# Optimization experiments

Measured on AMD Instinct MI355X. Metric: run time of the kernel, lower is better.

Reference implementation:

```python
import jax, jax.numpy as jnp
import numpy as np

D = 1024      # embedding_dim
H = 16        # n_heads
HD = D // H   # head_dim = 64
E = 8         # num_experts
K = 2         # top_k
I = 1024      # moe intermediate
S = 2048      # seq_len
B = 1
EPS = 1e-6
THETA = 10000.0


def _rmsnorm(x, w):
    xf = x.astype(jnp.float32)
    var = jnp.mean(xf * xf, axis=-1, keepdims=True)
    return (xf * jax.lax.rsqrt(var + EPS)).astype(x.dtype) * w


def _rope(x, positions):
    # x: [B, S, H, HD], neox-style rotate-half RoPE
    half = HD // 2
    inv_freq = 1.0 / (THETA ** (jnp.arange(0, half, dtype=jnp.float32) / half))
    freqs = positions.astype(jnp.float32)[:, None] * inv_freq[None, :]  # [S, half]
    cos = jnp.cos(freqs)[None, :, None, :]
    sin = jnp.sin(freqs)[None, :, None, :]
    x1, x2 = x[..., :half], x[..., half:]
    return jnp.concatenate([x1 * cos - x2 * sin, x1 * sin + x2 * cos], axis=-1).astype(x.dtype)


def _attn(x, positions, wqkv, wo):
    b, s, _ = x.shape
    qkv = (x @ wqkv).reshape(b, s, 3, H, HD)
    q, k, v = qkv[:, :, 0], qkv[:, :, 1], qkv[:, :, 2]
    q = _rope(q, positions)
    k = _rope(k, positions)
    scale = 1.0 / np.sqrt(HD)
    scores = jnp.einsum('bqhd,bkhd->bhqk', q, k) * scale
    causal = jnp.tril(jnp.ones((s, s), dtype=bool))
    scores = jnp.where(causal[None, None], scores, jnp.finfo(scores.dtype).min)
    probs = jax.nn.softmax(scores, axis=-1)
    o = jnp.einsum('bhqk,bkhd->bqhd', probs, v).reshape(b, s, D)
    return o @ wo


def _moe(x, gate_w, wg, wu, wd):
    # x: [T, D]
    T = x.shape[0]
    logits = x @ gate_w                                    # [T, E]
    probs = jax.nn.softmax(logits.astype(jnp.float32), axis=-1)
    vals, idx = jax.lax.top_k(probs, K)                    # [T, K]
    vals = vals / jnp.sum(vals, axis=-1, keepdims=True)    # renormalize=True
    combine = jnp.zeros((T, E), dtype=jnp.float32)
    combine = combine.at[jnp.arange(T)[:, None], idx].add(vals)
    combine = combine.astype(x.dtype)                      # [T, E]
    out = jnp.zeros_like(x)
    for e in range(E):  # fixed small expert loop; SwiGLU expert FFN
        h = jax.nn.silu(x @ wg[e]) * (x @ wu[e])
        out = out + combine[:, e:e + 1] * (h @ wd[e])
    return out


def setup_inputs() -> dict:
    key = jax.random.key(0)
    ks = jax.random.split(key, 8)
    std = 0.02
    return {
        'positions': jnp.arange(S, dtype=jnp.int32),
        'hidden_states': jax.random.normal(ks[0], (B, S, D), jnp.float32),
        'residual': jax.random.normal(ks[1], (B, S, D), jnp.float32),
        'ln1_w': jnp.ones((D,), jnp.float32),
        'ln2_w': jnp.ones((D,), jnp.float32),
        'wqkv': jax.random.normal(ks[2], (D, 3 * D), jnp.float32) * std,
        'wo': jax.random.normal(ks[3], (D, D), jnp.float32) * std,
        'gate_w': jax.random.normal(ks[4], (D, E), jnp.float32) * std,
        'wg': jax.random.normal(ks[5], (E, D, I), jnp.float32) * std,
        'wu': jax.random.normal(ks[6], (E, D, I), jnp.float32) * std,
        'wd': jax.random.normal(ks[7], (E, I, D), jnp.float32) * std,
    }


def reference(positions, hidden_states, residual, ln1_w, ln2_w, wqkv, wo, gate_w, wg, wu, wd):
    # _forward_with_post_attn_norm: residual arg is overwritten by hidden_states
    res = hidden_states
    x = _rmsnorm(hidden_states, ln1_w)
    x = res + _attn(x, positions, wqkv, wo)
    res2 = x
    y = _rmsnorm(x, ln2_w)
    b, s, _ = y.shape
    moe_out = _moe(y.reshape(-1, D), gate_w, wg, wu, wd).reshape(b, s, D)
    return res2 + moe_out
```

## Files before the change

### kernel.cpp

```cpp
#include <hip/hip_runtime.h>
#include <math.h>

constexpr int S  = 2048;
constexpr int D  = 1024;
constexpr int NH = 16;
constexpr int NE = 8;
constexpr float EPS   = 1e-6f;
constexpr float THETA = 10000.0f;
constexpr float SCL2  = 0.125f * 1.4426950408889634f;
constexpr float LOG2E = 1.4426950408889634f;

typedef unsigned short u16;
typedef unsigned int   u32;
typedef unsigned long long u64;
typedef __attribute__((ext_vector_type(8))) short short8;
typedef __attribute__((ext_vector_type(4))) float f32x4;

__device__ __forceinline__ u16 f2bf(float x) {
  union { float f; u32 u; } v; v.f = x;
  u32 r = (v.u + 0x7FFFu + ((v.u >> 16) & 1u)) >> 16;
  return (u16)r;
}
__device__ __forceinline__ float bf2f(u16 h) {
  union { u32 u; float f; } v; v.u = ((u32)h) << 16;
  return v.f;
}
__device__ __forceinline__ f32x4 mfma16(short8 a, short8 b, f32x4 c) {
  return __builtin_amdgcn_mfma_f32_16x16x32_bf16(a, b, c, 0, 0, 0);
}
__device__ __forceinline__ void gl_lds16(const void* g, void* l) {
  __builtin_amdgcn_global_load_lds((const __attribute__((address_space(1))) u32*)g,
                                   (__attribute__((address_space(3))) u32*)l, 16, 0, 0);
}
__device__ __forceinline__ u64 pack4bf(float a, float b, float c, float d) {
  return (u64)f2bf(a) | ((u64)f2bf(b) << 16) | ((u64)f2bf(c) << 32) | ((u64)f2bf(d) << 48);
}

__global__ __launch_bounds__(256) void prep_kernel(const float* __restrict__ wqkv,
    const float* __restrict__ wo, const float* __restrict__ wg, const float* __restrict__ wu,
    const float* __restrict__ wd, const int* __restrict__ positions,
    const float* __restrict__ hidden, const float* __restrict__ ln1_w,
    u16* __restrict__ wqkvT2, u16* __restrict__ woT2, u16* __restrict__ wgT,
    u16* __restrict__ wuT, u16* __restrict__ wdT, float2* __restrict__ ropetab,
    u16* __restrict__ xn2, int* __restrict__ counts) {
  const int b = blockIdx.x;
  const int tid = threadIdx.x;
  if (b >= 7424) {
    const int t = b - 7424;
    const float* xr = hidden + (size_t)t * D;
    float v[4]; float ss = 0.f;
#pragma unroll
    for (int i = 0; i < 4; ++i) { v[i] = xr[tid + i * 256]; ss += v[i] * v[i]; }
#pragma unroll
    for (int m = 32; m >= 1; m >>= 1) ss += __shfl_xor(ss, m, 64);
    __shared__ float red[4];
    if ((tid & 63) == 0) red[tid >> 6] = ss;
    __syncthreads();
    const float rs = rsqrtf((red[0] + red[1] + red[2] + red[3]) * (1.f / (float)D) + EPS);
#pragma unroll
    for (int i = 0; i < 4; ++i) {
      const int d = tid + i * 256;
      const float y = v[i] * rs * ln1_w[d];
      const u16 h = f2bf(y);
      xn2[(size_t)t * 2048 + d] = h;
      xn2[(size_t)t * 2048 + 1024 + d] = f2bf(y - bf2f(h));
    }
    return;
  }
  if (b >= 7168) {
    if (b == 7168 && tid < 8) counts[tid] = 0;
    const int idx = (b - 7168) * 256 + tid;
    const int t = idx >> 5, p = idx & 31;
    const float inv = powf(THETA, -(float)p * (1.f / 32.f));
    const float fr = (float)positions[t] * inv;
    float sn, cs; sincosf(fr, &sn, &cs);
    ropetab[idx] = make_float2(cs, sn);
    return;
  }
  __shared__ float t_[64][65];
  const float* W; u16* out; int N, n0, k0; bool split;
  if (b < 768) {
    W = wqkv; out = wqkvT2; N = 3072; split = true;
    n0 = (b % 48) * 64; k0 = (b / 48) * 64;
  } else if (b < 1024) {
    W = wo; out = woT2; N = 1024; split = true;
    const int r = b - 768; n0 = (r & 15) * 64; k0 = (r >> 4) * 64;
  } else {
    int r;
    if (b < 3072)      { r = b - 1024; const int e = r >> 8; W = wg + (size_t)e * 1048576; out = wgT + (size_t)e * 1048576; }
    else if (b < 5120) { r = b - 3072; const int e = r >> 8; W = wu + (size_t)e * 1048576; out = wuT + (size_t)e * 1048576; }
    else               { r = b - 5120; const int e = r >> 8; W = wd + (size_t)e * 1048576; out = wdT + (size_t)e * 1048576; }
    N = 1024; split = false;
    r &= 255; n0 = (r & 15) * 64; k0 = (r >> 4) * 64;
  }
  const int rr = tid >> 4, c4 = (tid & 15) * 4;
#pragma unroll
  for (int i = 0; i < 4; ++i) {
    const float4 v = *(const float4*)(W + (size_t)(k0 + rr + i * 16) * N + n0 + c4);
    t_[rr + i * 16][c4 + 0] = v.x; t_[rr + i * 16][c4 + 1] = v.y;
    t_[rr + i * 16][c4 + 2] = v.z; t_[rr + i * 16][c4 + 3] = v.w;
  }
  __syncthreads();
  if (split) {
#pragma unroll
    for (int i = 0; i < 4; ++i) {
      const int n = n0 + rr + i * 16;
      u16* oh = out + (size_t)n * 2048 + k0 + c4;
      const float v0 = t_[c4 + 0][rr + i * 16], v1 = t_[c4 + 1][rr + i * 16];
      const float v2 = t_[c4 + 2][rr + i * 16], v3 = t_[c4 + 3][rr + i * 16];
      *(u64*)(void*)oh = pack4bf(v0, v1, v2, v3);
      *(u64*)(void*)(oh + 1024) = pack4bf(v0 - bf2f(f2bf(v0)), v1 - bf2f(f2bf(v1)),
                                          v2 - bf2f(f2bf(v2)), v3 - bf2f(f2bf(v3)));
    }
  } else {
#pragma unroll
    for (int i = 0; i < 4; ++i) {
      const int n = n0 + rr + i * 16;
      u16* o = out + (size_t)n * 1024 + k0 + c4;
      *(u64*)(void*)o = pack4bf(t_[c4 + 0][rr + i * 16], t_[c4 + 1][rr + i * 16],
                                t_[c4 + 2][rr + i * 16], t_[c4 + 3][rr + i * 16]);
    }
  }
}

__global__ __launch_bounds__(256) void gemm_qkv(const u16* __restrict__ A2,
    const u16* __restrict__ Bt2, float* __restrict__ Cpart) {
  __shared__ u16 As[2][128 * 32];
  __shared__ u16 Bs[2][128 * 32];
  const int b = blockIdx.x;
  const int xcd = b & 7, ii = b >> 3;
  const int m0 = (ii & 15) * 128;
  const int np = (ii >> 4) % 3, ks = (ii >> 4) / 3;
  const int n0 = (xcd * 3 + np) * 128;
  const int kk0 = ks * 48, kk1 = kk0 + 48;
  const int tid = threadIdx.x, wv = tid >> 6, lane = tid & 63;
  const int l15 = lane & 15, lg = lane >> 4;
  const int wr = wv >> 1, wc = wv & 1;
  const int sr = lane >> 2, sk = (lane & 3) * 16;
  const u16* aptr[2]; const u16* bptr[2];
#pragma unroll
  for (int i = 0; i < 2; ++i) {
    aptr[i] = A2 + (size_t)(m0 + (wv * 2 + i) * 16 + sr) * 2048;
    bptr[i] = Bt2 + (size_t)(n0 + (wv * 2 + i) * 16 + sr) * 2048;
  }
  auto STAGE = [&](int buf, int kk) {
    const int t = kk * 32;
    int ka, kb;
    if (t < 1024)      { ka = t;        kb = t; }
    else if (t < 2048) { ka = t;        kb = t - 1024; }
    else               { ka = t - 2048; kb = t - 1024; }
#pragma unroll
    for (int i = 0; i < 2; ++i) {
      gl_lds16((const char*)(aptr[i] + ka) + sk, (char*)As + buf * 8192 + (wv * 2 + i) * 1024);
      gl_lds16((const char*)(bptr[i] + kb) + sk, (char*)Bs + buf * 8192 + (wv * 2 + i) * 1024);
    }
  };
  f32x4 acc[4][4] = {};
  STAGE(0, kk0);
  __syncthreads();
  int cur = 0;
  for (int kk = kk0; kk < kk1; ++kk) {
    if (kk + 1 < kk1) STAGE(cur ^ 1, kk + 1);
    const u16* Ab = (const u16*)As + cur * 4096;
    const u16* Bb = (const u16*)Bs + cur * 4096;
    short8 a[4], bb[4];
#pragma unroll
    for (int i = 0; i < 4; ++i)
      a[i] = *(const short8*)(const void*)(Ab + (size_t)(wr * 64 + i * 16 + l15) * 32 + lg * 8);
#pragma unroll
    for (int j = 0; j < 4; ++j)
      bb[j] = *(const short8*)(const void*)(Bb + (size_t)(wc * 64 + j * 16 + l15) * 32 + lg * 8);
    __builtin_amdgcn_s_setprio(1);
#pragma unroll
    for (int i = 0; i < 4; ++i)
#pragma unroll
      for (int j = 0; j < 4; ++j) acc[i][j] = mfma16(a[i], bb[j], acc[i][j]);
    __builtin_amdgcn_s_setprio(0);
    __syncthreads();
    cur ^= 1;
  }
  float* P = Cpart + (size_t)ks * S * 3072;
#pragma unroll
  for (int i = 0; i < 4; ++i)
#pragma unroll
    for (int j = 0; j < 4; ++j)
#pragma unroll
      for (int r = 0; r < 4; ++r) {
        const int row = m0 + wr * 64 + i * 16 + lg * 4 + r;
        const int col = n0 + wc * 64 + j * 16 + l15;
        P[(size_t)row * 3072 + col] = acc[i][j][r];
      }
}

__global__ __launch_bounds__(256) void qkv_combine(const float* __restrict__ Cp,
    const float2* __restrict__ tab, u16* __restrict__ Ch, u16* __restrict__ Cl) {
  const int t = blockIdx.x, tid = threadIdx.x;
  const float* r0 = Cp + (size_t)t * 3072;
  const float* r1 = r0 + (size_t)S * 3072;
  const size_t ob = (size_t)t * 3072;
#pragma unroll
  for (int i = 0; i < 4; ++i) {
    const int pi = tid + i * 256;
    const int h = pi >> 5, p = pi & 31;
    const int col = h * 64 + p;
    const float x1 = r0[col] + r1[col];
    const float x2 = r0[col + 32] + r1[col + 32];
    const float2 cs = tab[t * 32 + p];
    const float y1 = x1 * cs.x - x2 * cs.y;
    const float y2 = x1 * cs.y + x2 * cs.x;
    const u16 h1 = f2bf(y1);
    Ch[ob + col] = h1; Cl[ob + col] = f2bf(y1 - bf2f(h1));
    const u16 h2 = f2bf(y2);
    Ch[ob + col + 32] = h2; Cl[ob + col + 32] = f2bf(y2 - bf2f(h2));
  }
#pragma unroll
  for (int i = 0; i < 4; ++i) {
    const int col = 2048 + tid + i * 256;
    const float y = r0[col] + r1[col];
    const u16 h = f2bf(y);
    Ch[ob + col] = h; Cl[ob + col] = f2bf(y - bf2f(h));
  }
}

__global__ __launch_bounds__(256) void gemm_wo(const u16* __restrict__ A2,
    const u16* __restrict__ Bt2, float* __restrict__ Pout) {
  constexpr int N = 1024;
  __shared__ u16 As[2][128 * 32];
  __shared__ u16 Bs[2][128 * 32];
  const int b = blockIdx.x;
  const int xcd = b & 7, ii = b >> 3;
  const int n0 = xcd * 128;
  const int m0 = (ii & 15) * 128;
  const int ks = ii >> 4;
  const int kk0 = ks * 24, kk1 = kk0 + 24;
  const int tid = threadIdx.x, wv = tid >> 6, lane = tid & 63;
  const int l15 = lane & 15, lg = lane >> 4;
  const int wr = wv >> 1, wc = wv & 1;
  const int sr = lane >> 2, sk = (lane & 3) * 16;
  const u16* aptr[2]; const u16* bptr[2];
#pragma unroll
  for (int i = 0; i < 2; ++i) {
    aptr[i] = A2 + (size_t)(m0 + (wv * 2 + i) * 16 + sr) * 2048;
    bptr[i] = Bt2 + (size_t)(n0 + (wv * 2 + i) * 16 + sr) * 2048;
  }
  auto STAGE = [&](int buf, int kk) {
    const int t = kk * 32;
    int ka, kb;
    if (t < 1024)      { ka = t;        kb = t; }
    else if (t < 2048) { ka = t;        kb = t - 1024; }
    else               { ka = t - 2048; kb = t - 1024; }
#pragma unroll
    for (int i = 0; i < 2; ++i) {
      gl_lds16((const char*)(aptr[i] + ka) + sk, (char*)As + buf * 8192 + (wv * 2 + i) * 1024);
      gl_lds16((const char*)(bptr[i] + kb) + sk, (char*)Bs + buf * 8192 + (wv * 2 + i) * 1024);
    }
  };
  f32x4 acc[4][4] = {};
  STAGE(0, kk0);
  __syncthreads();
  int cur = 0;
  for (int kk = kk0; kk < kk1; ++kk) {
    if (kk + 1 < kk1) STAGE(cur ^ 1, kk + 1);
    const u16* Ab = (const u16*)As + cur * 4096;
    const u16* Bb = (const u16*)Bs + cur * 4096;
    short8 a[4], bb[4];
#pragma unroll
    for (int i = 0; i < 4; ++i)
      a[i] = *(const short8*)(const void*)(Ab + (size_t)(wr * 64 + i * 16 + l15) * 32 + lg * 8);
#pragma unroll
    for (int j = 0; j < 4; ++j)
      bb[j] = *(const short8*)(const void*)(Bb + (size_t)(wc * 64 + j * 16 + l15) * 32 + lg * 8);
    __builtin_amdgcn_s_setprio(1);
#pragma unroll
    for (int i = 0; i < 4; ++i)
#pragma unroll
      for (int j = 0; j < 4; ++j) acc[i][j] = mfma16(a[i], bb[j], acc[i][j]);
    __builtin_amdgcn_s_setprio(0);
    __syncthreads();
    cur ^= 1;
  }
  float* P = Pout + (size_t)ks * S * N;
#pragma unroll
  for (int i = 0; i < 4; ++i)
#pragma unroll
    for (int j = 0; j < 4; ++j)
#pragma unroll
      for (int r = 0; r < 4; ++r) {
        const int row = m0 + wr * 64 + i * 16 + lg * 4 + r;
        const int col = n0 + wc * 64 + j * 16 + l15;
        P[(size_t)row * N + col] = acc[i][j][r];
      }
}

__global__ __launch_bounds__(256, 3) void attn_mfma(const u16* __restrict__ Qh,
    const u16* __restrict__ Ql, float* __restrict__ Opart, float2* __restrict__ ml) {
  const int b = blockIdx.x;
  const int head = (b & 7) + 8 * ((b >> 3) & 1);
  const int qb = 31 - ((b >> 4) & 31);
  const int sp = (b >> 9) & 3;
  const int q0 = qb * 64;
  const int ktiles = qb + 1;
  const int kbase = ktiles >> 2, krem = ktiles & 3;
  const int t0 = sp * kbase + (sp < krem ? sp : krem);
  const int t1 = t0 + kbase + (sp < krem ? 1 : 0);
  const int tid = threadIdx.x, w = tid >> 6, lane = tid & 63;
  const int l15 = lane & 15, lg = lane >> 4;
  __shared__ u16 Kh[64 * 64];
  __shared__ u16 Kl[64 * 64];
  __shared__ __align__(16) u16 Vth[64 * 72];
  __shared__ __align__(16) u16 Vtl[64 * 72];
  __shared__ __align__(16) u16 Pp[4][16 * 72];

  short8 qh[2], qlo[2];
  {
    const size_t qbase = (size_t)(q0 + w * 16 + l15) * 3072 + head * 64;
    qh[0]  = *(const short8*)(const void*)(Qh + qbase + lg * 8);
    qh[1]  = *(const short8*)(const void*)(Qh + qbase + 32 + lg * 8);
    qlo[0] = *(const short8*)(const void*)(Ql + qbase + lg * 8);
    qlo[1] = *(const short8*)(const void*)(Ql + qbase + 32 + lg * 8);
  }
  f32x4 oacc[4] = {};
  float m_run = -__builtin_inff(), l_run = 0.f;
  const int qrow0 = q0 + w * 16 + lg * 4;
  const int qcol  = q0 + w * 16 + l15;

  const int vhl = tid >> 7, rem = tid & 127;
  const int vkq = rem & 15, vdg = rem >> 4;
  const u16* vbase = (vhl ? Ql : Qh) + 2048 + head * 64 + vdg * 8;
  u16* vdst = vhl ? Vtl : Vth;
  short8 vr[4];

  auto STAGEK = [&](int kt) {
#pragma unroll
    for (int i = 0; i < 2; ++i) {
      const int inst = w * 2 + i;
      const int key = inst * 8 + (lane >> 3);
      const int db = ((lane & 7) * 16) ^ ((key & 7) << 4);
      gl_lds16((const char*)(Qh + (size_t)(kt * 64 + key) * 3072 + 1024 + head * 64) + db,
               (char*)Kh + inst * 1024);
      gl_lds16((const char*)(Ql + (size_t)(kt * 64 + key) * 3072 + 1024 + head * 64) + db,
               (char*)Kl + inst * 1024);
    }
  };
  auto VLOAD = [&](int kt) {
    const u16* vs = vbase + (size_t)(kt * 64 + vkq * 4) * 3072;
    vr[0] = *(const short8*)(const void*)vs;
    vr[1] = *(const short8*)(const void*)(vs + 3072);
    vr[2] = *(const short8*)(const void*)(vs + 6144);
    vr[3] = *(const short8*)(const void*)(vs + 9216);
  };
  auto VWRITE = [&]() {
#pragma unroll
    for (int jj = 0; jj < 8; ++jj) {
      const u64 pk = (u64)(u16)vr[0][jj] | ((u64)(u16)vr[1][jj] << 16) |
                     ((u64)(u16)vr[2][jj] << 32) | ((u64)(u16)vr[3][jj] << 48);
      *(u64*)(void*)(vdst + (vdg * 8 + jj) * 72 + vkq * 4) = pk;
    }
  };

  if (t0 < t1) {
    STAGEK(t0);
    VLOAD(t0);
    VWRITE();
    __syncthreads();
  }
  for (int t = t0; t < t1; ++t) {
    const int k0 = t * 64;
    const bool more = (t + 1 < t1);
    f32x4 sacc[4];
    __builtin_amdgcn_s_setprio(1);
#pragma unroll
    for (int nt = 0; nt < 4; ++nt) {
      const int key = nt * 16 + l15;
      const char* kbh = (const char*)Kh + key * 128;
      const char* kbl = (const char*)Kl + key * 128;
      const int sw = (key & 7) << 4;
      const short8 kh0 = *(const short8*)(const void*)(kbh + ((lg * 16) ^ sw));
      const short8 kh1 = *(const short8*)(const void*)(kbh + ((64 + lg * 16) ^ sw));
      const short8 kl0 = *(const short8*)(const void*)(kbl + ((lg * 16) ^ sw));
      const short8 kl1 = *(const short8*)(const void*)(kbl + ((64 + lg * 16) ^ sw));
      f32x4 s = {};
      s = mfma16(kh0, qh[0], s);  s = mfma16(kh1, qh[1], s);
      s = mfma16(kh0, qlo[0], s); s = mfma16(kh1, qlo[1], s);
      s = mfma16(kl0, qh[0], s);  s = mfma16(kl1, qh[1], s);
      sacc[nt] = s;
    }
    __builtin_amdgcn_s_setprio(0);
    __syncthreads();
    if (more) { STAGEK(t + 1); VLOAD(t + 1); }
#pragma unroll
    for (int nt = 0; nt < 4; ++nt)
#pragma unroll
      for (int r = 0; r < 4; ++r) sacc[nt][r] *= SCL2;
    if (t == qb) {
#pragma unroll
      for (int nt = 0; nt < 4; ++nt) {
        const int keyb = k0 + nt * 16 + lg * 4;
#pragma unroll
        for (int r = 0; r < 4; ++r)
          if (keyb + r > qcol) sacc[nt][r] = -__builtin_inff();
      }
    }
    float mx = sacc[0][0];
#pragma unroll
    for (int nt = 0; nt < 4; ++nt)
#pragma unroll
      for (int r = 0; r < 4; ++r) mx = fmaxf(mx, sacc[nt][r]);
    mx = fmaxf(mx, __shfl_xor(mx, 16, 64));
    mx = fmaxf(mx, __shfl_xor(mx, 32, 64));
    const bool grow = mx > m_run + 8.f;
    if (__any(grow)) {
      const float m_new = fmaxf(m_run, mx);
      const float fac = __builtin_amdgcn_exp2f(m_run - m_new);
      m_run = m_new;
      l_run *= fac;
      float facB[4];
#pragma unroll
      for (int r = 0; r < 4; ++r) facB[r] = __shfl(fac, lg * 4 + r, 64);
#pragma unroll
      for (int nd = 0; nd < 4; ++nd)
#pragma unroll
        for (int r = 0; r < 4; ++r) oacc[nd][r] *= facB[r];
    }
    float ls = 0.f;
#pragma unroll
    for (int nt = 0; nt < 4; ++nt)
#pragma unroll
      for (int r = 0; r < 4; ++r) {
        sacc[nt][r] = __builtin_amdgcn_exp2f(sacc[nt][r] - m_run);
        ls += sacc[nt][r];
      }
    ls += __shfl_xor(ls, 16, 64);
    ls += __shfl_xor(ls, 32, 64);
    l_run += ls;
    u16* prow = &Pp[w][l15 * 72];
#pragma unroll
    for (int nt = 0; nt < 4; ++nt) {
      const u64 pk = (u64)(__float_as_uint(sacc[nt][0]) >> 16) |
                     ((u64)(__float_as_uint(sacc[nt][1]) >> 16) << 16) |
                     ((u64)(__float_as_uint(sacc[nt][2]) >> 16) << 32) |
                     ((u64)(__float_as_uint(sacc[nt][3]) >> 16) << 48);
      *(u64*)(void*)(prow + nt * 16 + lg * 4) = pk;
    }
    __builtin_amdgcn_s_setprio(1);
#pragma unroll
    for (int kk2 = 0; kk2 < 2; ++kk2) {
      const short8 pa = *(const short8*)(const void*)((const char*)prow + kk2 * 64 + lg * 16);
#pragma unroll
      for (int nd = 0; nd < 4; ++nd) {
        const short8 vbh = *(const short8*)(const void*)((const char*)Vth + (nd * 16 + l15) * 144 + kk2 * 64 + lg * 16);
        const short8 vbl = *(const short8*)(const void*)((const char*)Vtl + (nd * 16 + l15) * 144 + kk2 * 64 + lg * 16);
        oacc[nd] = mfma16(pa, vbh, oacc[nd]);
        oacc[nd] = mfma16(pa, vbl, oacc[nd]);
      }
    }
    __builtin_amdgcn_s_setprio(0);
    asm volatile("" ::: "memory");
#pragma unroll
    for (int nt = 0; nt < 4; ++nt) {
      float lo[4];
#pragma unroll
      for (int r = 0; r < 4; ++r)
        lo[r] = sacc[nt][r] - __uint_as_float(__float_as_uint(sacc[nt][r]) & 0xFFFF0000u);
      const u64 pk = (u64)(__float_as_uint(lo[0]) >> 16) |
                     ((u64)(__float_as_uint(lo[1]) >> 16) << 16) |
                     ((u64)(__float_as_uint(lo[2]) >> 16) << 32) |
                     ((u64)(__float_as_uint(lo[3]) >> 16) << 48);
      *(u64*)(void*)(prow + nt * 16 + lg * 4) = pk;
    }
    asm volatile("" ::: "memory");
    __builtin_amdgcn_s_setprio(1);
#pragma unroll
    for (int kk2 = 0; kk2 < 2; ++kk2) {
      const short8 pa = *(const short8*)(const void*)((const char*)prow + kk2 * 64 + lg * 16);
#pragma unroll
      for (int nd = 0; nd < 4; ++nd) {
        const short8 vbh = *(const short8*)(const void*)((const char*)Vth + (nd * 16 + l15) * 144 + kk2 * 64 + lg * 16);
        oacc[nd] = mfma16(pa, vbh, oacc[nd]);
      }
    }
    __builtin_amdgcn_s_setprio(0);
    __syncthreads();
    if (more) VWRITE();
  }
  float* Op = Opart + (size_t)sp * S * 1024;
#pragma unroll
  for (int nd = 0; nd < 4; ++nd)
#pragma unroll
    for (int r = 0; r < 4; ++r)
      Op[(size_t)(qrow0 + r) * 1024 + head * 64 + nd * 16 + l15] = oacc[nd][r];
  if (lg == 0) {
    ml[((size_t)sp * S + q0 + w * 16 + l15) * NH + head] = make_float2(m_run, l_run);
  }
}

__global__ __launch_bounds__(256) void attn_combine(const float* __restrict__ Op,
    const float2* __restrict__ ml, u16* __restrict__ OA2) {
  const int t = blockIdx.x, tid = threadIdx.x;
  const int h = tid >> 4, dq = (tid & 15) * 4;
  float2 a[4];
  float M = -__builtin_inff();
#pragma unroll
  for (int c = 0; c < 4; ++c) {
    a[c] = ml[((size_t)c * S + t) * NH + h];
    if (a[c].y > 0.f) M = fmaxf(M, a[c].x);
  }
  float e[4], denom = 0.f;
#pragma unroll
  for (int c = 0; c < 4; ++c) {
    e[c] = (a[c].y > 0.f) ? exp2f(a[c].x - M) : 0.f;
    denom += e[c] * a[c].y;
  }
  const float inv = 1.f / denom;
  float ov[4] = {0.f, 0.f, 0.f, 0.f};
#pragma unroll
  for (int c = 0; c < 4; ++c) {
    const float4 v = *(const float4*)(Op + ((size_t)c * S + t) * 1024 + h * 64 + dq);
    ov[0] += e[c] * v.x; ov[1] += e[c] * v.y; ov[2] += e[c] * v.z; ov[3] += e[c] * v.w;
  }
#pragma unroll
  for (int c2 = 0; c2 < 4; ++c2) {
    const float o = ov[c2] * inv;
    const size_t idx = (size_t)t * 2048 + h * 64 + dq + c2;
    const u16 hb = f2bf(o);
    OA2[idx] = hb;
    OA2[idx + 1024] = f2bf(o - bf2f(hb));
  }
}

__global__ __launch_bounds__(256) void rmsnorm_res2_gate(const float* __restrict__ hidden,
    const float* __restrict__ p01, const float* __restrict__ w2, const float* __restrict__ GW,
    float* __restrict__ out, u16* __restrict__ yb,
    int* __restrict__ counts, int* __restrict__ tok_map, float* __restrict__ w_map) {
  const int t = blockIdx.x;
  float v[4]; float ss = 0.f;
#pragma unroll
  for (int i = 0; i < 4; ++i) {
    const size_t idx = (size_t)t * D + threadIdx.x + i * 256;
    const float r = hidden[idx] + p01[idx] + p01[idx + (size_t)S * D] +
                    p01[idx + 2 * (size_t)S * D] + p01[idx + 3 * (size_t)S * D];
    v[i] = r; ss += r * r;
  }
#pragma unroll
  for (int m = 32; m >= 1; m >>= 1) ss += __shfl_xor(ss, m, 64);
  __shared__ float red[4];
  if ((threadIdx.x & 63) == 0) red[threadIdx.x >> 6] = ss;
  __syncthreads();
  const float rs = rsqrtf((red[0] + red[1] + red[2] + red[3]) * (1.f / (float)D) + EPS);
  float lg[8] = {};
#pragma unroll
  for (int i = 0; i < 4; ++i) {
    const int d = threadIdx.x + i * 256;
    const size_t idx = (size_t)t * D + d;
    const float y = v[i] * rs * w2[d];
    out[idx] = v[i];
    yb[idx] = f2bf(y);
    const float4 g0 = *(const float4*)(GW + d * 8);
    const float4 g1 = *(const float4*)(GW + d * 8 + 4);
    lg[0] += y * g0.x; lg[1] += y * g0.y; lg[2] += y * g0.z; lg[3] += y * g0.w;
    lg[4] += y * g1.x; lg[5] += y * g1.y; lg[6] += y * g1.z; lg[7] += y * g1.w;
  }
#pragma unroll
  for (int e = 0; e < 8; ++e)
#pragma unroll
    for (int m = 32; m >= 1; m >>= 1) lg[e] += __shfl_xor(lg[e], m, 64);
  __shared__ float wred[4][8];
  if ((threadIdx.x & 63) == 0)
#pragma unroll
    for (int e = 0; e < 8; ++e) wred[threadIdx.x >> 6][e] = lg[e];
  __syncthreads();
  if (threadIdx.x == 0) {
    float L[8];
#pragma unroll
    for (int e = 0; e < 8; ++e) L[e] = wred[0][e] + wred[1][e] + wred[2][e] + wred[3][e];
    int i0 = 0; float v0 = L[0];
    for (int i = 1; i < 8; ++i) if (L[i] > v0) { v0 = L[i]; i0 = i; }
    int i1 = -1; float v1 = -__builtin_inff();
    for (int i = 0; i < 8; ++i) if (i != i0 && L[i] > v1) { v1 = L[i]; i1 = i; }
    const float e1 = expf(v1 - v0);
    const float inv = 1.f / (1.f + e1);
    const int p0 = atomicAdd(&counts[i0], 1);
    tok_map[i0 * S + p0] = t;
    w_map[i0 * S + p0] = inv;
    const int p1 = atomicAdd(&counts[i1], 1);
    tok_map[i1 * S + p1] = t | 65536;
    w_map[i1 * S + p1] = e1 * inv;
  }
}

__global__ __launch_bounds__(256) void moe_gu(const u16* __restrict__ Yb,
    const u16* __restrict__ Wgb, const u16* __restrict__ Wub, u16* __restrict__ Hb,
    const int* __restrict__ counts, const int* __restrict__ tokmap) {
  const int b = blockIdx.x;
  const int e = b & 7, ii = b >> 3;
  const int n0 = (ii & 15) * 64;
  const int m0 = (ii >> 4) * 128;
  const int cnt = counts[e];
  if (m0 >= cnt) return;
  __shared__ u16 SH[2][16 * 512];
  const int tid = threadIdx.x, wv = tid >> 6, lane = tid & 63;
  const int l15 = lane & 15, lg = lane >> 4;
  const int wr = wv >> 1, wc = wv & 1;
  const int sr = lane >> 2, sk = (lane & 3) * 16;
  const u16* B1 = Wgb + (size_t)e * 1048576;
  const u16* B2 = Wub + (size_t)e * 1048576;
  const u16* cp[4];
#pragma unroll
  for (int i = 0; i < 4; ++i) {
    const int c = wv * 4 + i;
    if (c < 8) {
      const int arow = m0 + c * 16 + sr;
      const int tok = tokmap[e * S + arow] & 2047;
      cp[i] = Yb + (size_t)tok * 1024;
    } else if (c < 12) {
      cp[i] = B1 + (size_t)(n0 + (c - 8) * 16 + sr) * 1024;
    } else {
      cp[i] = B2 + (size_t)(n0 + (c - 12) * 16 + sr) * 1024;
    }
  }
  auto STAGE = [&](int buf, int k) {
#pragma unroll
    for (int i = 0; i < 4; ++i) {
      const int c = wv * 4 + i;
      gl_lds16((const char*)(cp[i] + k) + sk, (char*)SH + buf * 16384 + c * 1024);
    }
  };
  f32x4 acc1[4][2] = {};
  f32x4 acc2[4][2] = {};
  STAGE(0, 0);
  __syncthreads();
  int cur = 0;
  for (int kk = 0; kk < 32; ++kk) {
    if (kk < 31) STAGE(cur ^ 1, (kk + 1) * 32);
    const u16* Sb = (const u16*)SH + cur * 8192;
    short8 a[4], b1f[2], b2f[2];
#pragma unroll
    for (int i = 0; i < 4; ++i)
      a[i] = *(const short8*)(const void*)(Sb + (size_t)(wr * 64 + i * 16 + l15) * 32 + lg * 8);
#pragma unroll
    for (int j = 0; j < 2; ++j) {
      b1f[j] = *(const short8*)(const void*)(Sb + 4096 + (size_t)(wc * 32 + j * 16 + l15) * 32 + lg * 8);
      b2f[j] = *(const short8*)(const void*)(Sb + 6144 + (size_t)(wc * 32 + j * 16 + l15) * 32 + lg * 8);
    }
    __builtin_amdgcn_s_setprio(1);
#pragma unroll
    for (int i = 0; i < 4; ++i)
#pragma unroll
      for (int j = 0; j < 2; ++j) {
        acc1[i][j] = mfma16(a[i], b1f[j], acc1[i][j]);
        acc2[i][j] = mfma16(a[i], b2f[j], acc2[i][j]);
      }
    __builtin_amdgcn_s_setprio(0);
    __syncthreads();
    cur ^= 1;
  }
#pragma unroll
  for (int i = 0; i < 4; ++i)
#pragma unroll
    for (int j = 0; j < 2; ++j)
#pragma unroll
      for (int r = 0; r < 4; ++r) {
        const int row = m0 + wr * 64 + i * 16 + lg * 4 + r;
        if (row < cnt) {
          const float g = acc1[i][j][r];
          const float u = acc2[i][j][r];
          const float sig = __builtin_amdgcn_rcpf(1.f + __builtin_amdgcn_exp2f(-g * LOG2E));
          Hb[((size_t)e * 2048 + row) * 1024 + n0 + wc * 32 + j * 16 + l15] = f2bf(u * g * sig);
        }
      }
}

__global__ __launch_bounds__(256) void moe_down(const u16* __restrict__ Hb,
    const u16* __restrict__ Wdb, u16* __restrict__ slotp,
    const int* __restrict__ counts, const int* __restrict__ tokmap,
    const float* __restrict__ wmap) {
  const int b = blockIdx.x;
  const int e = b & 7, ii = b >> 3;
  const int m0 = (ii & 15) * 128;
  const int n0 = ((ii >> 4) & 7) * 128;
  const int ks = ii >> 7;
  const int cnt = counts[e];
  if (m0 >= cnt) return;
  __shared__ u16 As[2][128 * 32];
  __shared__ u16 Bs[2][128 * 32];
  const int tid = threadIdx.x, wv = tid >> 6, lane = tid & 63;
  const int l15 = lane & 15, lg = lane >> 4;
  const int wr = wv >> 1, wc = wv & 1;
  const int sr = lane >> 2, sk = (lane & 3) * 16;
  const u16* B = Wdb + (size_t)e * 1048576;
  const u16* aptr[2]; const u16* bptr[2];
#pragma unroll
  for (int i = 0; i < 2; ++i) {
    aptr[i] = Hb + ((size_t)e * 2048 + m0 + (wv * 2 + i) * 16 + sr) * 1024;
    bptr[i] = B + (size_t)(n0 + (wv * 2 + i) * 16 + sr) * 1024;
  }
  auto STAGE = [&](int buf, int k) {
#pragma unroll
    for (int i = 0; i < 2; ++i) {
      gl_lds16((const char*)(aptr[i] + k) + sk, (char*)As + buf * 8192 + (wv * 2 + i) * 1024);
      gl_lds16((const char*)(bptr[i] + k) + sk, (char*)Bs + buf * 8192 + (wv * 2 + i) * 1024);
    }
  };
  f32x4 acc[4][4] = {};
  const int kb0 = ks * 16, kb1 = kb0 + 16;
  STAGE(0, kb0 * 32);
  __syncthreads();
  int cur = 0;
  for (int kk = kb0; kk < kb1; ++kk) {
    if (kk + 1 < kb1) STAGE(cur ^ 1, (kk + 1) * 32);
    const u16* Ab = (const u16*)As + cur * 4096;
    const u16* Bb = (const u16*)Bs + cur * 4096;
    short8 a[4], bb[4];
#pragma unroll
    for (int i = 0; i < 4; ++i)
      a[i] = *(const short8*)(const void*)(Ab + (size_t)(wr * 64 + i * 16 + l15) * 32 + lg * 8);
#pragma unroll
    for (int j = 0; j < 4; ++j)
      bb[j] = *(const short8*)(const void*)(Bb + (size_t)(wc * 64 + j * 16 + l15) * 32 + lg * 8);
    __builtin_amdgcn_s_setprio(1);
#pragma unroll
    for (int i = 0; i < 4; ++i)
#pragma unroll
      for (int j = 0; j < 4; ++j) acc[i][j] = mfma16(a[i], bb[j], acc[i][j]);
    __builtin_amdgcn_s_setprio(0);
    __syncthreads();
    cur ^= 1;
  }
#pragma unroll
  for (int i = 0; i < 4; ++i)
#pragma unroll
    for (int j = 0; j < 4; ++j)
#pragma unroll
      for (int r = 0; r < 4; ++r) {
        const int row = m0 + wr * 64 + i * 16 + lg * 4 + r;
        if (row < cnt) {
          const int raw = tokmap[e * S + row];
          const int t = raw & 2047;
          const int sl = (raw >> 16) & 1;
          const float wgt = wmap[e * S + row];
          slotp[((size_t)(sl * 2 + ks) * S + t) * 1024 + n0 + wc * 64 + j * 16 + l15] =
              f2bf(wgt * acc[i][j][r]);
        }
      }
}

__global__ __launch_bounds__(256) void final_add(float* __restrict__ out,
    const u16* __restrict__ sp) {
  const size_t i = ((size_t)blockIdx.x * 256 + threadIdx.x) * 4;
  float4 o = *(float4*)(out + i);
#pragma unroll
  for (int c = 0; c < 4; ++c) {
    const u64 a = *(const u64*)(sp + (size_t)c * S * D + i);
    o.x += bf2f((u16)(a));
    o.y += bf2f((u16)(a >> 16));
    o.z += bf2f((u16)(a >> 32));
    o.w += bf2f((u16)(a >> 48));
  }
  *(float4*)(out + i) = o;
}

extern "C" void kernel_launch(void* const* d_in, const int* in_sizes, int n_in,
                              void* d_out, int out_size, void* d_ws, size_t ws_size,
                              hipStream_t stream) {
  const int*   positions = (const int*)d_in[0];
  const float* hidden    = (const float*)d_in[1];
  const float* ln1_w  = (const float*)d_in[3];
  const float* ln2_w  = (const float*)d_in[4];
  const float* wqkv   = (const float*)d_in[5];
  const float* wo     = (const float*)d_in[6];
  const float* gate_w = (const float*)d_in[7];
  const float* wg     = (const float*)d_in[8];
  const float* wu     = (const float*)d_in[9];
  const float* wd     = (const float*)d_in[10];
  float* out = (float*)d_out;

  char* ws = (char*)d_ws;
  const size_t MB = 1ull << 20;
  u16* wqkvT2 = (u16*)(ws);
  u16* QKVh   = (u16*)(ws);
  u16* OA2    = (u16*)(ws);
  u16* woT2   = (u16*)(ws + 12 * MB);
  u16* wgT    = (u16*)(ws + 16 * MB);
  u16* wuT    = (u16*)(ws + 32 * MB);
  u16* wdT    = (u16*)(ws + 48 * MB);
  float2* ropetab = (float2*)(ws + 64 * MB);
  float2* ml      = (float2*)(ws + 64 * MB + 524288);
  char* mapb = ws + 64 * MB + 1572864;
  int*   counts   = (int*)mapb;
  int*   tok_map  = (int*)(mapb + 8192);
  float* w_map    = (float*)(mapb + 8192 + 65536);
  u16* xn2    = (u16*)(ws + 66 * MB);
  u16* QKVl   = (u16*)(ws + 66 * MB);
  u16* yb     = (u16*)(ws + 66 * MB);
  float* Cpart  = (float*)(ws + 78 * MB);
  float* Opart  = (float*)(ws + 78 * MB);
  float* p01    = (float*)(ws + 78 * MB);
  u16* Hb     = (u16*)(ws + 78 * MB);
  u16* slotp  = (u16*)(ws + 110 * MB);

  prep_kernel<<<9472, 256, 0, stream>>>(wqkv, wo, wg, wu, wd, positions, hidden, ln1_w,
                                        wqkvT2, woT2, wgT, wuT, wdT, ropetab, xn2, counts);
  gemm_qkv<<<768, 256, 0, stream>>>(xn2, wqkvT2, Cpart);
  qkv_combine<<<S, 256, 0, stream>>>(Cpart, ropetab, QKVh, QKVl);
  attn_mfma<<<2048, 256, 0, stream>>>(QKVh, QKVl, Opart, ml);
  attn_combine<<<S, 256, 0, stream>>>(Opart, ml, OA2);
  gemm_wo<<<512, 256, 0, stream>>>(OA2, woT2, p01);
  rmsnorm_res2_gate<<<S, 256, 0, stream>>>(hidden, p01, ln2_w, gate_w, out, yb,
                                           counts, tok_map, w_map);
  moe_gu<<<2048, 256, 0, stream>>>(yb, wgT, wuT, Hb, counts, tok_map);
  moe_down<<<2048, 256, 0, stream>>>(Hb, wdT, slotp, counts, tok_map, w_map);
  final_add<<<2048, 256, 0, stream>>>(out, slotp);
}
```

Baseline: 308.5 us.

## Replace atomic expert routing with deterministic prefix-scan compaction kernel

The gate kernel no longer uses global atomics to append tokens to per-expert lists. It writes each token's top-2 experts and weights, and a new single-block kernel builds counts, token maps and weights with a packed 16-bit-lane prefix scan in token order. The rmsnorm/gate kernel is also vectorised to float4 loads and stores. This removes atomic contention and gives a sorted, deterministic token order, which may improve locality in the expert GEMMs. The cost is an extra serial single-block launch.

```diff
diff --git a/kernel.cpp b/kernel.cpp
--- a/kernel.cpp
+++ b/kernel.cpp
@@ -42,7 +42,7 @@
     const float* __restrict__ hidden, const float* __restrict__ ln1_w,
     u16* __restrict__ wqkvT2, u16* __restrict__ woT2, u16* __restrict__ wgT,
     u16* __restrict__ wuT, u16* __restrict__ wdT, float2* __restrict__ ropetab,
-    u16* __restrict__ xn2, int* __restrict__ counts) {
+    u16* __restrict__ xn2) {
   const int b = blockIdx.x;
   const int tid = threadIdx.x;
   if (b >= 7424) {
@@ -68,7 +68,6 @@
     return;
   }
   if (b >= 7168) {
-    if (b == 7168 && tid < 8) counts[tid] = 0;
     const int idx = (b - 7168) * 256 + tid;
     const int t = idx >> 5, p = idx & 31;
     const float inv = powf(THETA, -(float)p * (1.f / 32.f));
@@ -531,34 +530,35 @@
 __global__ __launch_bounds__(256) void rmsnorm_res2_gate(const float* __restrict__ hidden,
     const float* __restrict__ p01, const float* __restrict__ w2, const float* __restrict__ GW,
     float* __restrict__ out, u16* __restrict__ yb,
-    int* __restrict__ counts, int* __restrict__ tok_map, float* __restrict__ w_map) {
+    int* __restrict__ top2, float2* __restrict__ topw) {
   const int t = blockIdx.x;
-  float v[4]; float ss = 0.f;
-#pragma unroll
-  for (int i = 0; i < 4; ++i) {
-    const size_t idx = (size_t)t * D + threadIdx.x + i * 256;
-    const float r = hidden[idx] + p01[idx] + p01[idx + (size_t)S * D] +
-                    p01[idx + 2 * (size_t)S * D] + p01[idx + 3 * (size_t)S * D];
-    v[i] = r; ss += r * r;
-  }
+  const int d0 = threadIdx.x * 4;
+  const size_t base = (size_t)t * D + d0;
+  const float4 h4 = *(const float4*)(hidden + base);
+  const float4 a4 = *(const float4*)(p01 + base);
+  const float4 b4 = *(const float4*)(p01 + (size_t)S * D + base);
+  const float4 c4 = *(const float4*)(p01 + 2 * (size_t)S * D + base);
+  const float4 e4 = *(const float4*)(p01 + 3 * (size_t)S * D + base);
+  float v[4] = {h4.x + a4.x + b4.x + c4.x + e4.x, h4.y + a4.y + b4.y + c4.y + e4.y,
+                h4.z + a4.z + b4.z + c4.z + e4.z, h4.w + a4.w + b4.w + c4.w + e4.w};
+  float ss = v[0] * v[0] + v[1] * v[1] + v[2] * v[2] + v[3] * v[3];
 #pragma unroll
   for (int m = 32; m >= 1; m >>= 1) ss += __shfl_xor(ss, m, 64);
   __shared__ float red[4];
   if ((threadIdx.x & 63) == 0) red[threadIdx.x >> 6] = ss;
   __syncthreads();
   const float rs = rsqrtf((red[0] + red[1] + red[2] + red[3]) * (1.f / (float)D) + EPS);
+  const float4 w4 = *(const float4*)(w2 + d0);
+  const float y[4] = {v[0] * rs * w4.x, v[1] * rs * w4.y, v[2] * rs * w4.z, v[3] * rs * w4.w};
+  *(float4*)(out + base) = make_float4(v[0], v[1], v[2], v[3]);
+  *(u64*)(void*)(yb + base) = pack4bf(y[0], y[1], y[2], y[3]);
   float lg[8] = {};
 #pragma unroll
-  for (int i = 0; i < 4; ++i) {
-    const int d = threadIdx.x + i * 256;
-    const size_t idx = (size_t)t * D + d;
-    const float y = v[i] * rs * w2[d];
-    out[idx] = v[i];
-    yb[idx] = f2bf(y);
-    const float4 g0 = *(const float4*)(GW + d * 8);
-    const float4 g1 = *(const float4*)(GW + d * 8 + 4);
-    lg[0] += y * g0.x; lg[1] += y * g0.y; lg[2] += y * g0.z; lg[3] += y * g0.w;
-    lg[4] += y * g1.x; lg[5] += y * g1.y; lg[6] += y * g1.z; lg[7] += y * g1.w;
+  for (int j = 0; j < 4; ++j) {
+    const float4 g0 = *(const float4*)(GW + (d0 + j) * 8);
+    const float4 g1 = *(const float4*)(GW + (d0 + j) * 8 + 4);
+    lg[0] += y[j] * g0.x; lg[1] += y[j] * g0.y; lg[2] += y[j] * g0.z; lg[3] += y[j] * g0.w;
+    lg[4] += y[j] * g1.x; lg[5] += y[j] * g1.y; lg[6] += y[j] * g1.z; lg[7] += y[j] * g1.w;
   }
 #pragma unroll
   for (int e = 0; e < 8; ++e)
@@ -579,12 +579,59 @@
     for (int i = 0; i < 8; ++i) if (i != i0 && L[i] > v1) { v1 = L[i]; i1 = i; }
     const float e1 = expf(v1 - v0);
     const float inv = 1.f / (1.f + e1);
-    const int p0 = atomicAdd(&counts[i0], 1);
-    tok_map[i0 * S + p0] = t;
-    w_map[i0 * S + p0] = inv;
-    const int p1 = atomicAdd(&counts[i1], 1);
-    tok_map[i1 * S + p1] = t | 65536;
-    w_map[i1 * S + p1] = e1 * inv;
+    top2[t] = i0 | (i1 << 4);
+    topw[t] = make_float2(inv, e1 * inv);
+  }
+}
+
+__global__ __launch_bounds__(1024) void scatter_compact(const int* __restrict__ top2,
+    const float2* __restrict__ topw, int* __restrict__ counts,
+    int* __restrict__ tok_map, float* __restrict__ w_map) {
+  const int tid = threadIdx.x;
+  __shared__ u64 s0[1024], s1[1024];
+  int e_[2][2]; float w_[2][2];
+  u64 c0 = 0, c1 = 0;
+#pragma unroll
+  for (int k = 0; k < 2; ++k) {
+    const int t = tid * 2 + k;
+    const int pk = top2[t];
+    const float2 wv = topw[t];
+    e_[k][0] = pk & 15; e_[k][1] = (pk >> 4) & 15;
+    w_[k][0] = wv.x;    w_[k][1] = wv.y;
+#pragma unroll
+    for (int s = 0; s < 2; ++s) {
+      const int e = e_[k][s];
+      if (e < 4) c0 += 1ull << (e * 16); else c1 += 1ull << ((e - 4) * 16);
+    }
+  }
+  s0[tid] = c0; s1[tid] = c1;
+  __syncthreads();
+  for (int off = 1; off < 1024; off <<= 1) {
+    const u64 a0 = (tid >= off) ? s0[tid - off] : 0;
+    const u64 a1 = (tid >= off) ? s1[tid - off] : 0;
+    __syncthreads();
+    s0[tid] += a0; s1[tid] += a1;
+    __syncthreads();
+  }
+  if (tid == 1023) {
+#pragma unroll
+    for (int e = 0; e < 4; ++e) counts[e] = (int)((s0[1023] >> (e * 16)) & 0xFFFF);
+#pragma unroll
+    for (int e = 4; e < 8; ++e) counts[e] = (int)((s1[1023] >> ((e - 4) * 16)) & 0xFFFF);
+  }
+  u64 l0 = s0[tid] - c0, l1 = s1[tid] - c1;
+#pragma unroll
+  for (int k = 0; k < 2; ++k) {
+    const int t = tid * 2 + k;
+#pragma unroll
+    for (int s = 0; s < 2; ++s) {
+      const int e = e_[k][s];
+      int p;
+      if (e < 4) { p = (int)((l0 >> (e * 16)) & 0xFFFF); l0 += 1ull << (e * 16); }
+      else       { p = (int)((l1 >> ((e - 4) * 16)) & 0xFFFF); l1 += 1ull << ((e - 4) * 16); }
+      tok_map[e * S + p] = t | (s << 16);
+      w_map[e * S + p] = w_[k][s];
+    }
   }
 }
 
@@ -787,8 +834,10 @@
   float2* ml      = (float2*)(ws + 64 * MB + 524288);
   char* mapb = ws + 64 * MB + 1572864;
   int*   counts   = (int*)mapb;
-  int*   tok_map  = (int*)(mapb + 8192);
-  float* w_map    = (float*)(mapb + 8192 + 65536);
+  int*   tok_map  = (int*)(mapb + 512);
+  float* w_map    = (float*)(mapb + 512 + 65536);
+  int*   top2     = (int*)(mapb + 512 + 131072);
+  float2* topw    = (float2*)(mapb + 512 + 139264);
   u16* xn2    = (u16*)(ws + 66 * MB);
   u16* QKVl   = (u16*)(ws + 66 * MB);
   u16* yb     = (u16*)(ws + 66 * MB);
@@ -799,14 +848,14 @@
   u16* slotp  = (u16*)(ws + 110 * MB);
 
   prep_kernel<<<9472, 256, 0, stream>>>(wqkv, wo, wg, wu, wd, positions, hidden, ln1_w,
-                                        wqkvT2, woT2, wgT, wuT, wdT, ropetab, xn2, counts);
+                                        wqkvT2, woT2, wgT, wuT, wdT, ropetab, xn2);
   gemm_qkv<<<768, 256, 0, stream>>>(xn2, wqkvT2, Cpart);
   qkv_combine<<<S, 256, 0, stream>>>(Cpart, ropetab, QKVh, QKVl);
   attn_mfma<<<2048, 256, 0, stream>>>(QKVh, QKVl, Opart, ml);
   attn_combine<<<S, 256, 0, stream>>>(Opart, ml, OA2);
   gemm_wo<<<512, 256, 0, stream>>>(OA2, woT2, p01);
-  rmsnorm_res2_gate<<<S, 256, 0, stream>>>(hidden, p01, ln2_w, gate_w, out, yb,
-                                           counts, tok_map, w_map);
+  rmsnorm_res2_gate<<<S, 256, 0, stream>>>(hidden, p01, ln2_w, gate_w, out, yb, top2, topw);
+  scatter_compact<<<1, 1024, 0, stream>>>(top2, topw, counts, tok_map, w_map);
   moe_gu<<<2048, 256, 0, stream>>>(yb, wgT, wuT, Hb, counts, tok_map);
   moe_down<<<2048, 256, 0, stream>>>(Hb, wdT, slotp, counts, tok_map, w_map);
   final_add<<<2048, 256, 0, stream>>>(out, slotp);
```

Measured after the change: 277.4 us, median of 2. 1.11x faster.
